# Kernel optimization log

Measured on AMD Instinct MI355X. Metric: run time of the kernel, lower is better.

Reference implementation:

```python
import jax, jax.numpy as jnp
import numpy as np

B, DIM, H = 262144, 8, 100


def setup_inputs() -> dict:
    key = jax.random.key(0)
    ks = jax.random.split(key, 11)
    zt1 = jax.random.normal(ks[0], (B, DIM), dtype=jnp.float32)
    zt2 = zt1 + 0.05 * jax.random.normal(ks[1], (B, DIM), dtype=jnp.float32)
    dt = 0.01 * jnp.ones((B,), dtype=jnp.float32)
    s_in = 1.0 / np.sqrt(DIM)
    s_h = 1.0 / np.sqrt(H)
    # drift MLP: Linear(dim,100) -> Softplus -> Linear(100,dim)
    W1m = jax.random.normal(ks[2], (H, DIM), dtype=jnp.float32) * s_in
    b1m = jax.random.normal(ks[3], (H,), dtype=jnp.float32) * s_in
    W2m = jax.random.normal(ks[4], (DIM, H), dtype=jnp.float32) * s_h
    b2m = jax.random.normal(ks[5], (DIM,), dtype=jnp.float32) * s_h
    # diffusion net: Linear(dim,100) -> Softplus -> Linear(100,dim)  (diag=True -> n_entries=dim)
    W1d = jax.random.normal(ks[6], (H, DIM), dtype=jnp.float32) * s_in
    b1d = jax.random.normal(ks[7], (H,), dtype=jnp.float32) * s_in
    W2d = jax.random.normal(ks[8], (DIM, H), dtype=jnp.float32) * s_h
    b2d = jax.random.normal(ks[9], (DIM,), dtype=jnp.float32) * s_h
    return dict(zt1=zt1, zt2=zt2, dt=dt, W1m=W1m, b1m=b1m, W2m=W2m, b2m=b2m,
                W1d=W1d, b1d=b1d, W2d=W2d, b2d=b2d)


def reference(zt1, zt2, dt, W1m, b1m, W2m, b2m, W1d, b1d, W2d, b2d):
    dt0 = dt[0]
    # drift: mu = MLP(zt1) * dt
    mu = jnp.dot(jax.nn.softplus(jnp.dot(zt1, W1m.T) + b1m), W2m.T) + b2m  # [B, dim]
    mu = mu * dt0
    # diffusion: D = exp(Dnet(zt1)); diag Cholesky L = diag(D)
    D = jnp.exp(jnp.dot(jax.nn.softplus(jnp.dot(zt1, W1d.T) + b1d), W2d.T) + b2d)  # [B, dim]
    dz = zt2 - zt1
    # diag=True: cov = diag(D^2), precision = diag(1/D^2), logdet(cov) = 2*sum(log D)
    inv_var = 1.0 / (D * D)
    t1 = 2.0 * jnp.sum(jnp.log(D), axis=-1)
    t2 = jnp.sum(dz * dz * inv_var, axis=-1)
    t3 = -2.0 * jnp.sum(dz * mu * inv_var, axis=-1)
    t4 = jnp.sum(mu * mu * inv_var, axis=-1)
    const = jnp.asarray(-DIM / 2.0 * np.log(2.0 * np.pi), dtype=zt1.dtype)
    log_pz2 = const - 0.5 * (t1 + t2 + t3 + t4)
    loss = jnp.sum(-log_pz2)
    return loss, mu, D * jnp.sqrt(dt0)
```

## Files before the change

### kernel.cpp

```cpp
#include <hip/hip_runtime.h>

constexpr int BN = 262144;
constexpr int H_ = 100;

__device__ __forceinline__ float softplus_f(float x) {
    return __logf(1.0f + __expf(x));
}

__global__ __launch_bounds__(256) void sde_fused(
    const float* __restrict__ zt1, const float* __restrict__ zt2,
    const float* __restrict__ dtp,
    const float* __restrict__ W1m, const float* __restrict__ b1m,
    const float* __restrict__ W2m, const float* __restrict__ b2m,
    const float* __restrict__ W1d, const float* __restrict__ b1d,
    const float* __restrict__ W2d, const float* __restrict__ b2d,
    float* __restrict__ out)
{
    const int i = blockIdx.x * blockDim.x + threadIdx.x;
    const float dt0  = dtp[0];
    const float sqdt = sqrtf(dt0);

    float x[8];
    {
        const float4* p = reinterpret_cast<const float4*>(zt1) + (size_t)i * 2;
        float4 a = p[0], b = p[1];
        x[0]=a.x; x[1]=a.y; x[2]=a.z; x[3]=a.w;
        x[4]=b.x; x[5]=b.y; x[6]=b.z; x[7]=b.w;
    }

    float am[8], ad[8];
    #pragma unroll
    for (int k = 0; k < 8; ++k) { am[k] = b2m[k]; ad[k] = b2d[k]; }

    #pragma unroll 2
    for (int j = 0; j < H_; ++j) {
        float pm = b1m[j], pd = b1d[j];
        #pragma unroll
        for (int k = 0; k < 8; ++k) {
            pm = fmaf(x[k], W1m[j*8 + k], pm);
            pd = fmaf(x[k], W1d[j*8 + k], pd);
        }
        const float hm = softplus_f(pm);
        const float hd = softplus_f(pd);
        #pragma unroll
        for (int k = 0; k < 8; ++k) {
            am[k] = fmaf(hm, W2m[k*H_ + j], am[k]);
            ad[k] = fmaf(hd, W2d[k*H_ + j], ad[k]);
        }
    }

    float z2[8];
    {
        const float4* p = reinterpret_cast<const float4*>(zt2) + (size_t)i * 2;
        float4 a = p[0], b = p[1];
        z2[0]=a.x; z2[1]=a.y; z2[2]=a.z; z2[3]=a.w;
        z2[4]=b.x; z2[5]=b.y; z2[6]=b.z; z2[7]=b.w;
    }

    float t1 = 0.f, t2 = 0.f, t3 = 0.f, t4 = 0.f;
    float* __restrict__ mu_out = out + 1;
    float* __restrict__ sg_out = out + 1 + (size_t)BN * 8;
    #pragma unroll
    for (int k = 0; k < 8; ++k) {
        const float mu = am[k] * dt0;
        const float y  = ad[k];
        const float Dk = __expf(y);
        const float iv = __expf(-2.0f * y);
        const float dz = z2[k] - x[k];
        t1 += y;
        t2 = fmaf(dz * dz, iv, t2);
        t3 = fmaf(dz * mu, iv, t3);
        t4 = fmaf(mu * mu, iv, t4);
        mu_out[(size_t)i*8 + k] = mu;
        sg_out[(size_t)i*8 + k] = Dk * sqdt;
    }

    constexpr float NEG_CONST = 7.3515082656373808f;
    float nll = fmaf(0.5f, (2.0f*t1 + t2 - 2.0f*t3 + t4), NEG_CONST);

    #pragma unroll
    for (int off = 32; off > 0; off >>= 1) nll += __shfl_down(nll, off);

    __shared__ float wsum[4];
    const int lane = threadIdx.x & 63;
    const int wid  = threadIdx.x >> 6;
    if (lane == 0) wsum[wid] = nll;
    __syncthreads();
    if (threadIdx.x == 0) {
        atomicAdd(out, wsum[0] + wsum[1] + wsum[2] + wsum[3]);
    }
}

extern "C" void kernel_launch(void* const* d_in, const int* in_sizes, int n_in,
                              void* d_out, int out_size, void* d_ws, size_t ws_size,
                              hipStream_t stream) {
    hipMemsetAsync(d_out, 0, sizeof(float), stream);
    sde_fused<<<BN / 256, 256, 0, stream>>>(
        (const float*)d_in[0], (const float*)d_in[1], (const float*)d_in[2],
        (const float*)d_in[3], (const float*)d_in[4],
        (const float*)d_in[5], (const float*)d_in[6],
        (const float*)d_in[7], (const float*)d_in[8],
        (const float*)d_in[9], (const float*)d_in[10],
        (float*)d_out);
}
```

Before: 139.6 us.

## Split hidden dimension across wave pairs and combine partial sums via LDS

```diff
diff --git a/kernel.cpp b/kernel.cpp
--- a/kernel.cpp
+++ b/kernel.cpp
@@ -2,6 +2,7 @@
 
 constexpr int BN = 262144;
 constexpr int H_ = 100;
+constexpr int HHALF = 50;
 
 __device__ __forceinline__ float softplus_f(float x) {
     return __logf(1.0f + __expf(x));
@@ -16,24 +17,37 @@
     const float* __restrict__ W2d, const float* __restrict__ b2d,
     float* __restrict__ out)
 {
-    const int i = blockIdx.x * blockDim.x + threadIdx.x;
+    const int tid  = threadIdx.x;
+    const int lane = tid & 63;
+    const int wv   = tid >> 6;
+    const int pair = wv >> 1;
+    const int h    = __builtin_amdgcn_readfirstlane(wv & 1);
+    const int row  = blockIdx.x * 128 + pair * 64 + lane;
+
     const float dt0  = dtp[0];
     const float sqdt = sqrtf(dt0);
 
     float x[8];
     {
-        const float4* p = reinterpret_cast<const float4*>(zt1) + (size_t)i * 2;
+        const float4* p = reinterpret_cast<const float4*>(zt1) + (size_t)row * 2;
         float4 a = p[0], b = p[1];
         x[0]=a.x; x[1]=a.y; x[2]=a.z; x[3]=a.w;
         x[4]=b.x; x[5]=b.y; x[6]=b.z; x[7]=b.w;
     }
 
     float am[8], ad[8];
-    #pragma unroll
-    for (int k = 0; k < 8; ++k) { am[k] = b2m[k]; ad[k] = b2d[k]; }
+    if (h == 0) {
+        #pragma unroll
+        for (int k = 0; k < 8; ++k) { am[k] = b2m[k]; ad[k] = b2d[k]; }
+    } else {
+        #pragma unroll
+        for (int k = 0; k < 8; ++k) { am[k] = 0.f; ad[k] = 0.f; }
+    }
 
+    const int j0 = h * HHALF;
     #pragma unroll 2
-    for (int j = 0; j < H_; ++j) {
+    for (int jj = 0; jj < HHALF; ++jj) {
+        const int j = j0 + jj;
         float pm = b1m[j], pd = b1d[j];
         #pragma unroll
         for (int k = 0; k < 8; ++k) {
@@ -49,53 +63,67 @@
         }
     }
 
-    float z2[8];
-    {
-        const float4* p = reinterpret_cast<const float4*>(zt2) + (size_t)i * 2;
-        float4 a = p[0], b = p[1];
-        z2[0]=a.x; z2[1]=a.y; z2[2]=a.z; z2[3]=a.w;
-        z2[4]=b.x; z2[5]=b.y; z2[6]=b.z; z2[7]=b.w;
+    __shared__ float xch[256 * 9];
+    float* mine = &xch[tid * 9];
+    if (h == 0) {
+        mine[0]=am[4]; mine[1]=am[5]; mine[2]=am[6]; mine[3]=am[7];
+        mine[4]=ad[4]; mine[5]=ad[5]; mine[6]=ad[6]; mine[7]=ad[7];
+    } else {
+        mine[0]=am[0]; mine[1]=am[1]; mine[2]=am[2]; mine[3]=am[3];
+        mine[4]=ad[0]; mine[5]=ad[1]; mine[6]=ad[2]; mine[7]=ad[3];
+    }
+    __syncthreads();
+    const float* part = &xch[(tid ^ 64) * 9];
+
+    float* __restrict__ mu_out = out + 1;
+    float* __restrict__ sg_out = out + 1 + (size_t)BN * 8;
+
+    float t1 = 0.f, t2 = 0.f, t3 = 0.f, t4 = 0.f;
+
+#define EPI(K0)                                                              \
+    {                                                                        \
+        const float4 zb = *(reinterpret_cast<const float4*>(zt2) +           \
+                            ((size_t)row * 2 + (K0 / 4)));                   \
+        const float z2v[4] = {zb.x, zb.y, zb.z, zb.w};                       \
+        _Pragma("unroll")                                                    \
+        for (int q = 0; q < 4; ++q) {                                        \
+            const int k = K0 + q;                                            \
+            const float a_m = am[k] + part[q];                               \
+            const float a_d = ad[k] + part[4 + q];                           \
+            const float mu = a_m * dt0;                                      \
+            const float y  = a_d;                        \
+            const float Dk = __expf(y);                                      \
+            const float iv = __expf(-2.0f * y);                   \
+            const float dz = z2v[q] - x[k];                                  \
+            t1 += y;                                                         \
+            t2 = fmaf(dz * dz, iv, t2);                                      \
+            t3 = fmaf(dz * mu, iv, t3);                                      \
+            t4 = fmaf(mu * mu, iv, t4);                                      \
+            mu_out[(size_t)row * 8 + k] = mu;                                \
+            sg_out[(size_t)row * 8 + k] = Dk * sqdt;                         \
+        }                                                                    \
     }
 
-    float t1 = 0.f, t2 = 0.f, t3 = 0.f, t4 = 0.f;
-    float* __restrict__ mu_out = out + 1;
-    float* __restrict__ sg_out = out + 1 + (size_t)BN * 8;
-    #pragma unroll
-    for (int k = 0; k < 8; ++k) {
-        const float mu = am[k] * dt0;
-        const float y  = ad[k];
-        const float Dk = __expf(y);
-        const float iv = __expf(-2.0f * y);
-        const float dz = z2[k] - x[k];
-        t1 += y;
-        t2 = fmaf(dz * dz, iv, t2);
-        t3 = fmaf(dz * mu, iv, t3);
-        t4 = fmaf(mu * mu, iv, t4);
-        mu_out[(size_t)i*8 + k] = mu;
-        sg_out[(size_t)i*8 + k] = Dk * sqdt;
-    }
+    if (h == 0) { EPI(0) } else { EPI(4) }
+#undef EPI
 
-    constexpr float NEG_CONST = 7.3515082656373808f;
-    float nll = fmaf(0.5f, (2.0f*t1 + t2 - 2.0f*t3 + t4), NEG_CONST);
+    float nll = fmaf(0.5f, (2.0f * t1 + t2 - 2.0f * t3 + t4),
+                     3.67575413281869039f);
 
     #pragma unroll
     for (int off = 32; off > 0; off >>= 1) nll += __shfl_down(nll, off);
 
     __shared__ float wsum[4];
-    const int lane = threadIdx.x & 63;
-    const int wid  = threadIdx.x >> 6;
-    if (lane == 0) wsum[wid] = nll;
+    if (lane == 0) wsum[wv] = nll;
     __syncthreads();
-    if (threadIdx.x == 0) {
-        atomicAdd(out, wsum[0] + wsum[1] + wsum[2] + wsum[3]);
-    }
+    if (tid == 0) atomicAdd(out, wsum[0] + wsum[1] + wsum[2] + wsum[3]);
 }
 
 extern "C" void kernel_launch(void* const* d_in, const int* in_sizes, int n_in,
                               void* d_out, int out_size, void* d_ws, size_t ws_size,
                               hipStream_t stream) {
     hipMemsetAsync(d_out, 0, sizeof(float), stream);
-    sde_fused<<<BN / 256, 256, 0, stream>>>(
+    sde_fused<<<BN / 128, 256, 0, stream>>>(
         (const float*)d_in[0], (const float*)d_in[1], (const float*)d_in[2],
         (const float*)d_in[3], (const float*)d_in[4],
         (const float*)d_in[5], (const float*)d_in[6],
```

Measured after the change: 145.9 us. 1.05x slower.
